# Kernel optimization log

Hardware: AMD Instinct MI355X
Metric: run time of the kernel (lower is better)

Reference implementation:

```python
import jax, jax.numpy as jnp
import numpy as np

# Dims: B INRs, N probe points, d_in=2 coords, hidden H, out D_OUT, proj P
B, N, D_IN, H, D_OUT, P = 128, 4096, 2, 128, 3, 128
W0_SIREN = 30.0  # SIREN frequency scale
LN_EPS = 1e-5


def setup_inputs() -> dict:
    key = jax.random.key(0)
    ks = jax.random.split(key, 12)
    sn = lambda k, shape, sc: (jax.random.normal(k, shape, dtype=jnp.float32) * sc)
    return {
        # per-sample SIREN params, torch layout: weight [b, in, out, 1], bias [b, out, 1]
        "w0": sn(ks[0], (B, D_IN, H, 1), 1.0 / D_IN),
        "w1": sn(ks[1], (B, H, H, 1), np.sqrt(6.0 / H) / W0_SIREN),
        "w2": sn(ks[2], (B, H, D_OUT, 1), np.sqrt(6.0 / H) / W0_SIREN),
        "b0": sn(ks[3], (B, H, 1), 0.1),
        "b1": sn(ks[4], (B, H, 1), 0.1),
        "b2": sn(ks[5], (B, D_OUT, 1), 0.1),
        # learned probe coordinates, initialized U[-1, 1) as in the module
        "inputs": jax.random.uniform(ks[6], (1, N, D_IN), dtype=jnp.float32, minval=-1.0, maxval=1.0),
        # projection (num_inputs -> proj_dim) + LayerNorm params, one per probed layer (4 total)
        "pw": sn(ks[7], (4, N, P), 1.0 / np.sqrt(N)),
        "pb": jnp.zeros((4, P), jnp.float32),
        "ln_g": jnp.ones((4, P), jnp.float32),
        "ln_b": jnp.zeros((4, P), jnp.float32),
    }


def _layernorm(x, g, b):
    m = jnp.mean(x, axis=-1, keepdims=True)
    v = jnp.mean(jnp.square(x - m), axis=-1, keepdims=True)
    return (x - m) * jax.lax.rsqrt(v + LN_EPS) * g + b


def reference(w0, w1, w2, b0, b1, b2, inputs, pw, pb, ln_g, ln_b):
    b = w0.shape[0]
    x = jnp.broadcast_to(inputs, (b,) + inputs.shape[1:])  # [b, n, d_in]

    def lin(h, W, bb):
        # per-sample linear: [b,n,i] @ [b,i,o] + [b,1,o]
        return jnp.einsum('bni,bio->bno', h, W[..., 0]) + bb[:, None, :, 0]

    h1 = jnp.sin(W0_SIREN * lin(x, w0, b0))   # [b, n, H]
    h2 = jnp.sin(W0_SIREN * lin(h1, w1, b1))  # [b, n, H]
    h3 = lin(h2, w2, b2)                      # [b, n, D_OUT] (last layer: no sine)
    feats = [x, h1, h2, h3]  # probe features per node layer (input coords + activations)

    outs = []
    for i, f in enumerate(feats):
        # permute to [b, dim_i, n], project n -> P, then LayerNorm over P
        z = jnp.einsum('bnd,np->bdp', f, pw[i]) + pb[i]
        outs.append(_layernorm(z, ln_g[i], ln_b[i]))
    return jnp.concatenate(outs, axis=1)  # [b, d_in + H + H + D_OUT, P]
```

## Files before the change

### kernel.cpp

```cpp
#include <hip/hip_runtime.h>
#include <hip/hip_bf16.h>


typedef unsigned short u16;
typedef __attribute__((ext_vector_type(8))) short short8;
typedef __attribute__((ext_vector_type(4))) short short4v;
typedef __attribute__((ext_vector_type(4))) float f32x4;
typedef __attribute__((ext_vector_type(4))) float float4v;

#define DEV __device__ __forceinline__

#define KSC 4.7746482927568605f

DEV float b2f(u16 h){ return __uint_as_float(((unsigned)h) << 16); }
DEV u16 f2b(float f){
  unsigned u = __float_as_uint(f);
  return (u16)((u + 0x7FFFu + ((u >> 16) & 1u)) >> 16);
}
DEV u16 f2b_hw(float f){
  __hip_bfloat16 h = __float2bfloat16(f);
  return __builtin_bit_cast(unsigned short, h);
}
DEV float sin_rev(float r){
#if __has_builtin(__builtin_amdgcn_sinf)
  return __builtin_amdgcn_sinf(r);
#else
  return __sinf(r * 6.283185307179586f);
#endif
}
template<int C> DEV float dpp_add(float x){
  int yi = __builtin_amdgcn_update_dpp(0, __float_as_int(x), C, 0xF, 0xF, true);
  return x + __int_as_float(yi);
}
DEV float sum16(float x){
  x = dpp_add<0x128>(x); x = dpp_add<0x124>(x);
  x = dpp_add<0x122>(x); x = dpp_add<0x121>(x);
  return x;
}

DEV int is_bf16_fmt(const void* lng){ return *(const unsigned*)lng == 0x3F803F80u; }
struct In {
  const float* f; const u16* h; int bf;
  DEV In(const void* p, int b_) : f((const float*)p), h((const u16*)p), bf(b_) {}
  DEV float at(size_t i) const { return bf ? b2f(h[i]) : f[i]; }
};

__global__ __launch_bounds__(256) void k_prep(const void* pwv, const void* inpv,
                                              const void* lngv,
                                              u16* __restrict__ pwT2,
                                              float* __restrict__ xbuf,
                                              float* __restrict__ zpart){
  const int bf = is_bf16_fmt(lngv);
  const int t = threadIdx.x;
  if (blockIdx.x == 256){
    In inp(inpv, bf);
    for (int i = t; i < 8192; i += 256) xbuf[i] = inp.at(i);
    return;
  }
  In pw(pwv, bf);
  const int layer = blockIdx.x >> 6;
  const int nc = blockIdx.x & 63;
  const int n0 = nc * 64;

  if (layer == 0){
    In inp(inpv, bf);
    const int d = t >> 7, p = t & 127;
    float s = 0.f;
#pragma unroll 8
    for (int k = 0; k < 64; k++)
      s = fmaf(inp.at((size_t)(n0 + k) * 2 + d),
               pw.at((size_t)(n0 + k) * 128 + p), s);
    zpart[(size_t)nc * 384 + d * 128 + p] = s;
    return;
  }

  __shared__ u16 tile[64 * 129];
  const size_t base = ((size_t)layer * 4096 + n0) * 128;
#pragma unroll
  for (int k = 0; k < 32; k++){
    int idx = k * 256 + t, n = idx >> 7, p = idx & 127;
    tile[n * 129 + p] = f2b(pw.at(base + (size_t)n * 128 + p));
  }
  if (layer == 3 && t < 128){
    float s = 0.f;
#pragma unroll 8
    for (int k = 0; k < 64; k++)
      s += pw.at(base + (size_t)k * 128 + t);
    zpart[(size_t)nc * 384 + 256 + t] = s;
  }
  __syncthreads();
  u16* dst = pwT2 + ((size_t)(layer - 1) * 128 + nc * 2) * 4096;
#pragma unroll
  for (int k = 0; k < 32; k++){
    int o = k * 256 + t;
    int frag = (o >> 3) & 511, j = o & 7;
    int p = ((frag >> 6) << 4) | ((frag >> 2) & 15);
    int nn = ((o >> 12) << 5) | ((frag & 3) << 3) | j;
    dst[o] = tile[nn * 129 + p];
  }
}

__global__ __launch_bounds__(384)
void k_zs2(const float* __restrict__ zpart, float* __restrict__ zs){
  const int t = threadIdx.x;
  float s = 0.f;
  for (int c = 0; c < 64; c++) s += zpart[(size_t)c * 384 + t];
  zs[t] = s;
}

#define S_NK 136
#define S_T  40

template<bool PARTIAL>
__global__ __launch_bounds__(512, 2)
void k_main(const void* w0v, const void* w1v, const void* w2v,
            const void* b0v, const void* b1v, const void* b2v,
            const void* pbv, const void* lgv, const void* lbv,
            const u16* __restrict__ pwTg, const float* __restrict__ xbuf,
            const float* __restrict__ zs,
            float* __restrict__ outp, int TS){
  __shared__ __align__(16) u16 sh1nk[32 * S_NK];
  __shared__ __align__(16) u16 sh1T[128 * S_T];
  __shared__ __align__(16) u16 sh2T[2][128 * S_T];
  __shared__ float sW2[512];
  __shared__ float sb2[4];
  __shared__ float sPB[512], sG[512], sBB[512];

  float* sP1 = (float*)sh1nk;
  float* sP2 = (float*)sh1T;
  float* sM  = (float*)sh2T;
  float* sI  = (float*)sh2T + 512;

  const int bf = is_bf16_fmt(lgv);
  In w0(w0v, bf), w1(w1v, bf), w2(w2v, bf), b0(b0v, bf), b1(b1v, bf),
     b2(b2v, bf), pb(pbv, bf), lg(lgv, bf), lb(lbv, bf);

  const int t = threadIdx.x;
  const int b = blockIdx.x & 127, sseg = blockIdx.x >> 7;
  const int lane = t & 63, wave = t >> 6, quad = lane >> 4, r16 = lane & 15;
  const int oo = wave * 16 + r16;

  if (t >= 256 && t < 384){
    int i = t - 256;
    sW2[i * 4 + 0] = w2.at(((size_t)b * 128 + i) * 3 + 0);
    sW2[i * 4 + 1] = w2.at(((size_t)b * 128 + i) * 3 + 1);
    sW2[i * 4 + 2] = w2.at(((size_t)b * 128 + i) * 3 + 2);
    sW2[i * 4 + 3] = 0.f;
  }
  if (t < 4) sb2[t] = (t < 3) ? b2.at(b * 3 + t) : 0.f;
  sPB[t] = pb.at(t); sG[t] = lg.at(t); sBB[t] = lb.at(t);

  const int p1n = t >> 4, p1hb = (t & 15) * 8;
  float w00[8], w01[8], b00[8];
#pragma unroll
  for (int j = 0; j < 8; j++){
    w00[j] = w0.at((size_t)b * 256 + p1hb + j) * KSC;
    w01[j] = w0.at((size_t)b * 256 + 128 + p1hb + j) * KSC;
    b00[j] = b0.at((size_t)b * 128 + p1hb + j) * KSC;
  }
  const int p2h = t & 127, p2nb = (t >> 7) * 8;
  const float q00 = w0.at((size_t)b * 256 + p2h) * KSC;
  const float q01 = w0.at((size_t)b * 256 + 128 + p2h) * KSC;
  const float qb0 = b0.at((size_t)b * 128 + p2h) * KSC;
  const float bias1k = b1.at((size_t)b * 128 + oo) * KSC;

  short8 w1f[4];
#pragma unroll
  for (int ks = 0; ks < 4; ks++){
#pragma unroll
    for (int j = 0; j < 8; j++)
      w1f[ks][j] = (short)f2b(w1.at((size_t)b * 16384 +
                                    (size_t)(ks * 32 + quad * 8 + j) * 128 + oo));
  }

  const int frag = wave * 64 + r16 * 4 + quad;
  const u16* bsrc = pwTg + (size_t)frag * 8;

  const f32x4 zz = {0.f,0.f,0.f,0.f};
  f32x4 az1[8], az2[8], ay[8];
#pragma unroll
  for (int i = 0; i < 8; i++){ az1[i] = zz; az2[i] = zz; ay[i] = zz; }

  const int nb0 = sseg * TS;
  short8 bbc[3];
#pragma unroll
  for (int L = 0; L < 3; L++)
    bbc[L] = *(const short8*)(bsrc + ((size_t)L * 128 + nb0) * 4096);
  short8 bb2p = bbc[1], bb3p = bbc[2];
  float2 xp1 = *(const float2*)(xbuf + (size_t)(nb0 * 32 + p1n) * 2);

  __syncthreads();

  int cb = 0;
  for (int nt = 0; nt < TS; nt++){
    const int n0 = (sseg * TS + nt) * 32;

    float4v xq[4];
#pragma unroll
    for (int q = 0; q < 4; q++)
      xq[q] = *(const float4v*)(xbuf + (size_t)(n0 + p2nb) * 2 + q * 4);
    {
      short8 v;
#pragma unroll
      for (int j = 0; j < 8; j++){
        float a = fmaf(xp1.y, w01[j], fmaf(xp1.x, w00[j], b00[j]));
        a -= rintf(a);
        v[j] = (short)f2b_hw(sin_rev(a));
      }
      *(short8*)&sh1nk[p1n * S_NK + p1hb] = v;
    }
    {
      short8 v;
#pragma unroll
      for (int j = 0; j < 8; j++){
        float x0 = xq[j >> 1][(j & 1) * 2], x1 = xq[j >> 1][(j & 1) * 2 + 1];
        float a = fmaf(x1, q01, fmaf(x0, q00, qb0));
        a -= rintf(a);
        v[j] = (short)f2b_hw(sin_rev(a));
      }
      *(short8*)&sh1T[p2h * S_T + p2nb] = v;
    }
    if (nt){
      const u16* s2p = sh2T[cb ^ 1];
#pragma unroll
      for (int mb = 0; mb < 8; mb++){
        short8 a = *(const short8*)&s2p[(mb * 16 + r16) * S_T + quad * 8];
        az2[mb] = __builtin_amdgcn_mfma_f32_16x16x32_bf16(a, bb2p, az2[mb], 0, 0, 0);
        ay[mb]  = __builtin_amdgcn_mfma_f32_16x16x32_bf16(a, bb3p, ay[mb], 0, 0, 0);
      }
    }
    __syncthreads();

    {
      const int nn = (nt + 1 < TS) ? nt + 1 : nt;
      const int nbn = sseg * TS + nn;
      short8 bbn[3];
#pragma unroll
      for (int L = 0; L < 3; L++)
        bbn[L] = *(const short8*)(bsrc + ((size_t)L * 128 + nbn) * 4096);
      float2 xp1n = *(const float2*)(xbuf + (size_t)(nbn * 32 + p1n) * 2);

      f32x4 h0 = zz, h1a = zz;
#pragma unroll
      for (int ks = 0; ks < 4; ks++){
        h0  = __builtin_amdgcn_mfma_f32_16x16x32_bf16(
                *(short8*)&sh1nk[r16 * S_NK + ks * 32 + quad * 8], w1f[ks], h0, 0, 0, 0);
        h1a = __builtin_amdgcn_mfma_f32_16x16x32_bf16(
                *(short8*)&sh1nk[(16 + r16) * S_NK + ks * 32 + quad * 8], w1f[ks], h1a, 0, 0, 0);
      }
#pragma unroll
      for (int mb = 0; mb < 8; mb++)
        az1[mb] = __builtin_amdgcn_mfma_f32_16x16x32_bf16(
                    *(short8*)&sh1T[(mb * 16 + r16) * S_T + quad * 8],
                    bbc[0], az1[mb], 0, 0, 0);
      {
        short4v v;
#pragma unroll
        for (int r = 0; r < 4; r++){
          float a = fmaf(h0[r], KSC, bias1k); a -= rintf(a);
          v[r] = (short)f2b_hw(sin_rev(a));
        }
        *(short4v*)&sh2T[cb][oo * S_T + quad * 4] = v;
#pragma unroll
        for (int r = 0; r < 4; r++){
          float a = fmaf(h1a[r], KSC, bias1k); a -= rintf(a);
          v[r] = (short)f2b_hw(sin_rev(a));
        }
        *(short4v*)&sh2T[cb][oo * S_T + 16 + quad * 4] = v;
      }

      bb2p = bbc[1]; bb3p = bbc[2];
#pragma unroll
      for (int L = 0; L < 3; L++) bbc[L] = bbn[L];
      xp1 = xp1n;
    }
    __syncthreads();
    cb ^= 1;
  }

  {
    const u16* s2p = sh2T[cb ^ 1];
#pragma unroll
    for (int mb = 0; mb < 8; mb++){
      short8 a = *(const short8*)&s2p[(mb * 16 + r16) * S_T + quad * 8];
      az2[mb] = __builtin_amdgcn_mfma_f32_16x16x32_bf16(a, bb2p, az2[mb], 0, 0, 0);
      ay[mb]  = __builtin_amdgcn_mfma_f32_16x16x32_bf16(a, bb3p, ay[mb], 0, 0, 0);
    }
  }

  const int p = oo;
  float z3v[3];
#pragma unroll
  for (int d = 0; d < 3; d++){
    float a = 0.f;
#pragma unroll
    for (int mb = 0; mb < 8; mb++)
#pragma unroll
      for (int r = 0; r < 4; r++)
        a = fmaf(sW2[(mb * 16 + quad * 4 + r) * 4 + d], ay[mb][r], a);
    a += __shfl_xor(a, 16, 64); a += __shfl_xor(a, 32, 64);
    z3v[d] = a;
  }
  if (!PARTIAL){
    const float S3v = zs[256 + p];
#pragma unroll
    for (int d = 0; d < 3; d++) z3v[d] += sb2[d] * S3v;
  }

  if (PARTIAL){
    float* zp = outp + ((size_t)(sseg * 128 + b)) * 261 * 128;
    if (quad == 0){
#pragma unroll
      for (int d = 0; d < 3; d++) zp[(size_t)(258 + d) * 128 + p] = z3v[d];
    }
#pragma unroll
    for (int mb = 0; mb < 8; mb++)
#pragma unroll
      for (int r = 0; r < 4; r++){
        int drow = mb * 16 + quad * 4 + r;
        zp[(size_t)(2 + drow) * 128 + p]   = az1[mb][r];
        zp[(size_t)(130 + drow) * 128 + p] = az2[mb][r];
      }
    return;
  }

  const float pb0v = sPB[p],       pb1v = sPB[128 + p];
  const float pb2v = sPB[256 + p], pb3v = sPB[384 + p];

  auto rowsum = [&](float v, int row, bool wr){
    float s1 = sum16(v), s2 = sum16(v * v);
    if (wr && r16 == 0){ sP1[row * 8 + wave] = s1; sP2[row * 8 + wave] = s2; }
  };
#pragma unroll
  for (int mb = 0; mb < 8; mb++)
#pragma unroll
    for (int r = 0; r < 4; r++)
      rowsum(az1[mb][r] + pb1v, 2 + mb * 16 + quad * 4 + r, true);
#pragma unroll
  for (int mb = 0; mb < 8; mb++)
#pragma unroll
    for (int r = 0; r < 4; r++)
      rowsum(az2[mb][r] + pb2v, 130 + mb * 16 + quad * 4 + r, true);
#pragma unroll
  for (int d = 0; d < 3; d++) rowsum(z3v[d] + pb3v, 258 + d, quad == 0);
  __syncthreads();

  if (t < 2){
    float s1 = 0.f, s2 = 0.f;
    for (int pp = 0; pp < 128; pp++){
      float v = zs[t * 128 + pp] + sPB[pp];
      s1 += v; s2 += v * v;
    }
    float m = s1 * (1.f / 128.f);
    float var = fmaf(-m, m, s2 * (1.f / 128.f));
    sM[t] = m;
    sI[t] = rsqrtf(fmaxf(var, 0.f) + 1e-5f);
  } else if (t < 261){
    float s1 = 0.f, s2 = 0.f;
#pragma unroll
    for (int w = 0; w < 8; w++){ s1 += sP1[t * 8 + w]; s2 += sP2[t * 8 + w]; }
    float m = s1 * (1.f / 128.f);
    float var = fmaf(-m, m, s2 * (1.f / 128.f));
    sM[t] = m;
    sI[t] = rsqrtf(fmaxf(var, 0.f) + 1e-5f);
  }
  __syncthreads();

  const size_t ob = (size_t)b * 261 * 128;
  auto emit = [&](float v, int row, int grp){
    outp[ob + (size_t)row * 128 + p] =
      (v - sM[row]) * sI[row] * sG[grp * 128 + p] + sBB[grp * 128 + p];
  };
  if (quad == 0){
#pragma unroll
    for (int r = 0; r < 2; r++) emit(zs[r * 128 + p] + pb0v, r, 0);
#pragma unroll
    for (int d = 0; d < 3; d++) emit(z3v[d] + pb3v, 258 + d, 3);
  }
#pragma unroll
  for (int mb = 0; mb < 8; mb++)
#pragma unroll
    for (int r = 0; r < 4; r++)
      emit(az1[mb][r] + pb1v, 2 + mb * 16 + quad * 4 + r, 1);
#pragma unroll
  for (int mb = 0; mb < 8; mb++)
#pragma unroll
    for (int r = 0; r < 4; r++)
      emit(az2[mb][r] + pb2v, 130 + mb * 16 + quad * 4 + r, 2);
}

__global__ __launch_bounds__(256)
void k_ln(const float* __restrict__ zp, const void* pbv, const void* lgv,
          const void* lbv, const void* b2v, const float* __restrict__ zpart,
          float* __restrict__ out, int split){
  const int bf = is_bf16_fmt(lgv);
  In pb(pbv, bf), lg(lgv, bf), lb(lbv, bf), b2(b2v, bf);
  const int lane = threadIdx.x & 63;
  const int row = blockIdx.x * 4 + (threadIdx.x >> 6);
  const int b = row / 261, d = row % 261;
  const int grp = (d < 2) ? 0 : (d < 130) ? 1 : (d < 258) ? 2 : 3;
  const int p0 = lane * 2;
  float v0 = pb.at(grp * 128 + p0), v1 = pb.at(grp * 128 + p0 + 1);
  if (d < 2){
    float s0 = 0.f, s1z = 0.f;
    for (int c = 0; c < 64; c++){
      s0  += zpart[(size_t)c * 384 + d * 128 + p0];
      s1z += zpart[(size_t)c * 384 + d * 128 + p0 + 1];
    }
    v0 += s0;
    v1 += s1z;
  } else {
    for (int s2 = 0; s2 < split; s2++){
      const float* zr = zp + ((size_t)(s2 * 128 + b) * 261 + d) * 128;
      v0 += zr[p0]; v1 += zr[p0 + 1];
    }
    if (d >= 258){
      float s0 = 0.f, s1z = 0.f;
      for (int c = 0; c < 64; c++){
        s0  += zpart[(size_t)c * 384 + 256 + p0];
        s1z += zpart[(size_t)c * 384 + 256 + p0 + 1];
      }
      float bb = b2.at((size_t)b * 3 + (d - 258));
      v0 = fmaf(bb, s0, v0);
      v1 = fmaf(bb, s1z, v1);
    }
  }
  float s1 = v0 + v1, s2s = v0 * v0 + v1 * v1;
#pragma unroll
  for (int o = 1; o < 64; o <<= 1){
    s1 += __shfl_xor(s1, o, 64);
    s2s += __shfl_xor(s2s, o, 64);
  }
  float m = s1 * (1.f / 128.f);
  float var = fmaf(-m, m, s2s * (1.f / 128.f));
  float inv = rsqrtf(fmaxf(var, 0.f) + 1e-5f);
  float2 o2;
  o2.x = (v0 - m) * inv * lg.at(grp * 128 + p0)     + lb.at(grp * 128 + p0);
  o2.y = (v1 - m) * inv * lg.at(grp * 128 + p0 + 1) + lb.at(grp * 128 + p0 + 1);
  *(float2*)(out + (size_t)row * 128 + p0) = o2;
}

extern "C" void kernel_launch(void* const* d_in, const int* in_sizes, int n_in,
                              void* d_out, int out_size, void* d_ws, size_t ws_size,
                              hipStream_t stream){
  const void* w0  = d_in[0];
  const void* w1  = d_in[1];
  const void* w2  = d_in[2];
  const void* b0  = d_in[3];
  const void* b1  = d_in[4];
  const void* b2  = d_in[5];
  const void* inp = d_in[6];
  const void* pw  = d_in[7];
  const void* pb  = d_in[8];
  const void* lng = d_in[9];
  const void* lnb = d_in[10];
  float* out = (float*)d_out;

  char* ws = (char*)d_ws;
  u16* pwT2    = (u16*)ws;
  float* xbuf  = (float*)(ws + 3145728);
  float* zs    = (float*)(ws + 3145728 + 32768);
  float* zpart = (float*)(ws + 3145728 + 32768 + 2048);
  const size_t zoff = 3145728 + 32768 + 2048 + 98304;
  float* zp = (float*)(ws + zoff);
  const size_t seg = (size_t)128 * 261 * 128 * 4;

  const int split = (ws_size >= zoff + 2 * seg) ? 2 : 1;

  k_prep<<<257, 256, 0, stream>>>(pw, inp, lng, pwT2, xbuf, zpart);
  if (split == 2){
    k_main<true><<<256, 512, 0, stream>>>(w0, w1, w2, b0, b1, b2,
        pb, lng, lnb, pwT2, xbuf, zs, zp, 64);
    k_ln<<<(128 * 261) / 4, 256, 0, stream>>>(zp, pb, lng, lnb, b2, zpart, out, 2);
  } else {
    k_zs2<<<1, 384, 0, stream>>>(zpart, zs);
    k_main<false><<<128, 512, 0, stream>>>(w0, w1, w2, b0, b1, b2,
        pb, lng, lnb, pwT2, xbuf, zs, out, 128);
  }
}
```

Before: 218.6 us.

## Retile main MFMA loop to 2x4 wave grid and always use separate LN kernel

Each wave now owns a 64-row by 32-column tile, using two B fragments per layer, instead of a full 128-row strip with one fragment. Each A fragment read from shared memory now feeds two MFMAs, which roughly halves LDS A-fragment reads at the cost of twice the global B loads. The fused LayerNorm path inside k_main is removed, so k_main always writes partial projections that k_ln normalises, including the split=1 case. The z3 contributions are reduced across the two row-waves through shared memory.

```diff
diff --git a/kernel.cpp b/kernel.cpp
--- a/kernel.cpp
+++ b/kernel.cpp
@@ -27,15 +27,6 @@
 #else
   return __sinf(r * 6.283185307179586f);
 #endif
-}
-template<int C> DEV float dpp_add(float x){
-  int yi = __builtin_amdgcn_update_dpp(0, __float_as_int(x), C, 0xF, 0xF, true);
-  return x + __int_as_float(yi);
-}
-DEV float sum16(float x){
-  x = dpp_add<0x128>(x); x = dpp_add<0x124>(x);
-  x = dpp_add<0x122>(x); x = dpp_add<0x121>(x);
-  return x;
 }
 
 DEV int is_bf16_fmt(const void* lng){ return *(const unsigned*)lng == 0x3F803F80u; }
@@ -100,45 +91,29 @@
   }
 }
 
-__global__ __launch_bounds__(384)
-void k_zs2(const float* __restrict__ zpart, float* __restrict__ zs){
-  const int t = threadIdx.x;
-  float s = 0.f;
-  for (int c = 0; c < 64; c++) s += zpart[(size_t)c * 384 + t];
-  zs[t] = s;
-}
-
 #define S_NK 136
 #define S_T  40
 
-template<bool PARTIAL>
 __global__ __launch_bounds__(512, 2)
 void k_main(const void* w0v, const void* w1v, const void* w2v,
-            const void* b0v, const void* b1v, const void* b2v,
-            const void* pbv, const void* lgv, const void* lbv,
+            const void* b0v, const void* b1v, const void* lgv,
             const u16* __restrict__ pwTg, const float* __restrict__ xbuf,
-            const float* __restrict__ zs,
             float* __restrict__ outp, int TS){
   __shared__ __align__(16) u16 sh1nk[32 * S_NK];
   __shared__ __align__(16) u16 sh1T[128 * S_T];
   __shared__ __align__(16) u16 sh2T[2][128 * S_T];
   __shared__ float sW2[512];
-  __shared__ float sb2[4];
-  __shared__ float sPB[512], sG[512], sBB[512];
-
-  float* sP1 = (float*)sh1nk;
-  float* sP2 = (float*)sh1T;
-  float* sM  = (float*)sh2T;
-  float* sI  = (float*)sh2T + 512;
+
+  float* sZ3 = (float*)sh1nk;
 
   const int bf = is_bf16_fmt(lgv);
-  In w0(w0v, bf), w1(w1v, bf), w2(w2v, bf), b0(b0v, bf), b1(b1v, bf),
-     b2(b2v, bf), pb(pbv, bf), lg(lgv, bf), lb(lbv, bf);
+  In w0(w0v, bf), w1(w1v, bf), w2(w2v, bf), b0(b0v, bf), b1(b1v, bf);
 
   const int t = threadIdx.x;
   const int b = blockIdx.x & 127, sseg = blockIdx.x >> 7;
   const int lane = t & 63, wave = t >> 6, quad = lane >> 4, r16 = lane & 15;
   const int oo = wave * 16 + r16;
+  const int wr = wave >> 2, wc = wave & 3;
 
   if (t >= 256 && t < 384){
     int i = t - 256;
@@ -147,8 +122,6 @@
     sW2[i * 4 + 2] = w2.at(((size_t)b * 128 + i) * 3 + 2);
     sW2[i * 4 + 3] = 0.f;
   }
-  if (t < 4) sb2[t] = (t < 3) ? b2.at(b * 3 + t) : 0.f;
-  sPB[t] = pb.at(t); sG[t] = lg.at(t); sBB[t] = lb.at(t);
 
   const int p1n = t >> 4, p1hb = (t & 15) * 8;
   float w00[8], w01[8], b00[8];
@@ -173,8 +146,8 @@
                                     (size_t)(ks * 32 + quad * 8 + j) * 128 + oo));
   }
 
-  const int frag = wave * 64 + r16 * 4 + quad;
-  const u16* bsrc = pwTg + (size_t)frag * 8;
+  const u16* bsrc0 = pwTg + (size_t)((wc * 2    ) * 64 + r16 * 4 + quad) * 8;
+  const u16* bsrc1 = pwTg + (size_t)((wc * 2 + 1) * 64 + r16 * 4 + quad) * 8;
 
   const f32x4 zz = {0.f,0.f,0.f,0.f};
   f32x4 az1[8], az2[8], ay[8];
@@ -182,11 +155,14 @@
   for (int i = 0; i < 8; i++){ az1[i] = zz; az2[i] = zz; ay[i] = zz; }
 
   const int nb0 = sseg * TS;
-  short8 bbc[3];
-#pragma unroll
-  for (int L = 0; L < 3; L++)
-    bbc[L] = *(const short8*)(bsrc + ((size_t)L * 128 + nb0) * 4096);
-  short8 bb2p = bbc[1], bb3p = bbc[2];
+  short8 bbc[3][2];
+#pragma unroll
+  for (int L = 0; L < 3; L++){
+    bbc[L][0] = *(const short8*)(bsrc0 + ((size_t)L * 128 + nb0) * 4096);
+    bbc[L][1] = *(const short8*)(bsrc1 + ((size_t)L * 128 + nb0) * 4096);
+  }
+  short8 bb2p0 = bbc[1][0], bb2p1 = bbc[1][1];
+  short8 bb3p0 = bbc[2][0], bb3p1 = bbc[2][1];
   float2 xp1 = *(const float2*)(xbuf + (size_t)(nb0 * 32 + p1n) * 2);
 
   __syncthreads();
@@ -223,10 +199,12 @@
     if (nt){
       const u16* s2p = sh2T[cb ^ 1];
 #pragma unroll
-      for (int mb = 0; mb < 8; mb++){
-        short8 a = *(const short8*)&s2p[(mb * 16 + r16) * S_T + quad * 8];
-        az2[mb] = __builtin_amdgcn_mfma_f32_16x16x32_bf16(a, bb2p, az2[mb], 0, 0, 0);
-        ay[mb]  = __builtin_amdgcn_mfma_f32_16x16x32_bf16(a, bb3p, ay[mb], 0, 0, 0);
+      for (int m = 0; m < 4; m++){
+        short8 a = *(const short8*)&s2p[(wr * 64 + m * 16 + r16) * S_T + quad * 8];
+        az2[m*2+0] = __builtin_amdgcn_mfma_f32_16x16x32_bf16(a, bb2p0, az2[m*2+0], 0, 0, 0);
+        az2[m*2+1] = __builtin_amdgcn_mfma_f32_16x16x32_bf16(a, bb2p1, az2[m*2+1], 0, 0, 0);
+        ay[m*2+0]  = __builtin_amdgcn_mfma_f32_16x16x32_bf16(a, bb3p0, ay[m*2+0], 0, 0, 0);
+        ay[m*2+1]  = __builtin_amdgcn_mfma_f32_16x16x32_bf16(a, bb3p1, ay[m*2+1], 0, 0, 0);
       }
     }
     __syncthreads();
@@ -234,10 +212,12 @@
     {
       const int nn = (nt + 1 < TS) ? nt + 1 : nt;
       const int nbn = sseg * TS + nn;
-      short8 bbn[3];
-#pragma unroll
-      for (int L = 0; L < 3; L++)
-        bbn[L] = *(const short8*)(bsrc + ((size_t)L * 128 + nbn) * 4096);
+      short8 bbn[3][2];
+#pragma unroll
+      for (int L = 0; L < 3; L++){
+        bbn[L][0] = *(const short8*)(bsrc0 + ((size_t)L * 128 + nbn) * 4096);
+        bbn[L][1] = *(const short8*)(bsrc1 + ((size_t)L * 128 + nbn) * 4096);
+      }
       float2 xp1n = *(const float2*)(xbuf + (size_t)(nbn * 32 + p1n) * 2);
 
       f32x4 h0 = zz, h1a = zz;
@@ -249,10 +229,11 @@
                 *(short8*)&sh1nk[(16 + r16) * S_NK + ks * 32 + quad * 8], w1f[ks], h1a, 0, 0, 0);
       }
 #pragma unroll
-      for (int mb = 0; mb < 8; mb++)
-        az1[mb] = __builtin_amdgcn_mfma_f32_16x16x32_bf16(
-                    *(short8*)&sh1T[(mb * 16 + r16) * S_T + quad * 8],
-                    bbc[0], az1[mb], 0, 0, 0);
+      for (int m = 0; m < 4; m++){
+        short8 a = *(const short8*)&sh1T[(wr * 64 + m * 16 + r16) * S_T + quad * 8];
+        az1[m*2+0] = __builtin_amdgcn_mfma_f32_16x16x32_bf16(a, bbc[0][0], az1[m*2+0], 0, 0, 0);
+        az1[m*2+1] = __builtin_amdgcn_mfma_f32_16x16x32_bf16(a, bbc[0][1], az1[m*2+1], 0, 0, 0);
+      }
       {
         short4v v;
 #pragma unroll
@@ -269,9 +250,10 @@
         *(short4v*)&sh2T[cb][oo * S_T + 16 + quad * 4] = v;
       }
 
-      bb2p = bbc[1]; bb3p = bbc[2];
-#pragma unroll
-      for (int L = 0; L < 3; L++) bbc[L] = bbn[L];
+      bb2p0 = bbc[1][0]; bb2p1 = bbc[1][1];
+      bb3p0 = bbc[2][0]; bb3p1 = bbc[2][1];
+#pragma unroll
+      for (int L = 0; L < 3; L++){ bbc[L][0] = bbn[L][0]; bbc[L][1] = bbn[L][1]; }
       xp1 = xp1n;
     }
     __syncthreads();
@@ -281,112 +263,57 @@
   {
     const u16* s2p = sh2T[cb ^ 1];
 #pragma unroll
-    for (int mb = 0; mb < 8; mb++){
-      short8 a = *(const short8*)&s2p[(mb * 16 + r16) * S_T + quad * 8];
-      az2[mb] = __builtin_amdgcn_mfma_f32_16x16x32_bf16(a, bb2p, az2[mb], 0, 0, 0);
-      ay[mb]  = __builtin_amdgcn_mfma_f32_16x16x32_bf16(a, bb3p, ay[mb], 0, 0, 0);
-    }
-  }
-
-  const int p = oo;
-  float z3v[3];
-#pragma unroll
-  for (int d = 0; d < 3; d++){
-    float a = 0.f;
-#pragma unroll
-    for (int mb = 0; mb < 8; mb++)
-#pragma unroll
-      for (int r = 0; r < 4; r++)
-        a = fmaf(sW2[(mb * 16 + quad * 4 + r) * 4 + d], ay[mb][r], a);
-    a += __shfl_xor(a, 16, 64); a += __shfl_xor(a, 32, 64);
-    z3v[d] = a;
-  }
-  if (!PARTIAL){
-    const float S3v = zs[256 + p];
-#pragma unroll
-    for (int d = 0; d < 3; d++) z3v[d] += sb2[d] * S3v;
-  }
-
-  if (PARTIAL){
-    float* zp = outp + ((size_t)(sseg * 128 + b)) * 261 * 128;
-    if (quad == 0){
-#pragma unroll
-      for (int d = 0; d < 3; d++) zp[(size_t)(258 + d) * 128 + p] = z3v[d];
-    }
-#pragma unroll
-    for (int mb = 0; mb < 8; mb++)
+    for (int m = 0; m < 4; m++){
+      short8 a = *(const short8*)&s2p[(wr * 64 + m * 16 + r16) * S_T + quad * 8];
+      az2[m*2+0] = __builtin_amdgcn_mfma_f32_16x16x32_bf16(a, bb2p0, az2[m*2+0], 0, 0, 0);
+      az2[m*2+1] = __builtin_amdgcn_mfma_f32_16x16x32_bf16(a, bb2p1, az2[m*2+1], 0, 0, 0);
+      ay[m*2+0]  = __builtin_amdgcn_mfma_f32_16x16x32_bf16(a, bb3p0, ay[m*2+0], 0, 0, 0);
+      ay[m*2+1]  = __builtin_amdgcn_mfma_f32_16x16x32_bf16(a, bb3p1, ay[m*2+1], 0, 0, 0);
+    }
+  }
+
+  float z3p[3][2];
+#pragma unroll
+  for (int dd = 0; dd < 3; dd++){
+#pragma unroll
+    for (int n = 0; n < 2; n++){
+      float a = 0.f;
+#pragma unroll
+      for (int m = 0; m < 4; m++)
+#pragma unroll
+        for (int r = 0; r < 4; r++)
+          a = fmaf(sW2[(wr * 64 + m * 16 + quad * 4 + r) * 4 + dd], ay[m*2+n][r], a);
+      a += __shfl_xor(a, 16, 64); a += __shfl_xor(a, 32, 64);
+      z3p[dd][n] = a;
+    }
+  }
+  if (lane < 16){
+#pragma unroll
+    for (int dd = 0; dd < 3; dd++)
+#pragma unroll
+      for (int n = 0; n < 2; n++)
+        sZ3[((wr * 4 + wc) * 3 + dd) * 32 + n * 16 + r16] = z3p[dd][n];
+  }
+
+  float* zp = outp + ((size_t)(sseg * 128 + b)) * 261 * 128;
+#pragma unroll
+  for (int m = 0; m < 4; m++)
+#pragma unroll
+    for (int n = 0; n < 2; n++)
 #pragma unroll
       for (int r = 0; r < 4; r++){
-        int drow = mb * 16 + quad * 4 + r;
-        zp[(size_t)(2 + drow) * 128 + p]   = az1[mb][r];
-        zp[(size_t)(130 + drow) * 128 + p] = az2[mb][r];
-      }
-    return;
-  }
-
-  const float pb0v = sPB[p],       pb1v = sPB[128 + p];
-  const float pb2v = sPB[256 + p], pb3v = sPB[384 + p];
-
-  auto rowsum = [&](float v, int row, bool wr){
-    float s1 = sum16(v), s2 = sum16(v * v);
-    if (wr && r16 == 0){ sP1[row * 8 + wave] = s1; sP2[row * 8 + wave] = s2; }
-  };
-#pragma unroll
-  for (int mb = 0; mb < 8; mb++)
-#pragma unroll
-    for (int r = 0; r < 4; r++)
-      rowsum(az1[mb][r] + pb1v, 2 + mb * 16 + quad * 4 + r, true);
-#pragma unroll
-  for (int mb = 0; mb < 8; mb++)
-#pragma unroll
-    for (int r = 0; r < 4; r++)
-      rowsum(az2[mb][r] + pb2v, 130 + mb * 16 + quad * 4 + r, true);
-#pragma unroll
-  for (int d = 0; d < 3; d++) rowsum(z3v[d] + pb3v, 258 + d, quad == 0);
+        int drow = wr * 64 + m * 16 + quad * 4 + r;
+        int pcol = wc * 32 + n * 16 + r16;
+        zp[(size_t)(2 + drow) * 128 + pcol]   = az1[m*2+n][r];
+        zp[(size_t)(130 + drow) * 128 + pcol] = az2[m*2+n][r];
+      }
   __syncthreads();
-
-  if (t < 2){
-    float s1 = 0.f, s2 = 0.f;
-    for (int pp = 0; pp < 128; pp++){
-      float v = zs[t * 128 + pp] + sPB[pp];
-      s1 += v; s2 += v * v;
-    }
-    float m = s1 * (1.f / 128.f);
-    float var = fmaf(-m, m, s2 * (1.f / 128.f));
-    sM[t] = m;
-    sI[t] = rsqrtf(fmaxf(var, 0.f) + 1e-5f);
-  } else if (t < 261){
-    float s1 = 0.f, s2 = 0.f;
-#pragma unroll
-    for (int w = 0; w < 8; w++){ s1 += sP1[t * 8 + w]; s2 += sP2[t * 8 + w]; }
-    float m = s1 * (1.f / 128.f);
-    float var = fmaf(-m, m, s2 * (1.f / 128.f));
-    sM[t] = m;
-    sI[t] = rsqrtf(fmaxf(var, 0.f) + 1e-5f);
-  }
-  __syncthreads();
-
-  const size_t ob = (size_t)b * 261 * 128;
-  auto emit = [&](float v, int row, int grp){
-    outp[ob + (size_t)row * 128 + p] =
-      (v - sM[row]) * sI[row] * sG[grp * 128 + p] + sBB[grp * 128 + p];
-  };
-  if (quad == 0){
-#pragma unroll
-    for (int r = 0; r < 2; r++) emit(zs[r * 128 + p] + pb0v, r, 0);
-#pragma unroll
-    for (int d = 0; d < 3; d++) emit(z3v[d] + pb3v, 258 + d, 3);
-  }
-#pragma unroll
-  for (int mb = 0; mb < 8; mb++)
-#pragma unroll
-    for (int r = 0; r < 4; r++)
-      emit(az1[mb][r] + pb1v, 2 + mb * 16 + quad * 4 + r, 1);
-#pragma unroll
-  for (int mb = 0; mb < 8; mb++)
-#pragma unroll
-    for (int r = 0; r < 4; r++)
-      emit(az2[mb][r] + pb2v, 130 + mb * 16 + quad * 4 + r, 2);
+  if (t < 384){
+    int dd = t >> 7, p = t & 127, wcc = p >> 5, pl = p & 31;
+    float v = sZ3[((0 * 4 + wcc) * 3 + dd) * 32 + pl]
+            + sZ3[((1 * 4 + wcc) * 3 + dd) * 32 + pl];
+    zp[(size_t)(258 + dd) * 128 + p] = v;
+  }
 }
 
 __global__ __launch_bounds__(256)
@@ -459,22 +386,15 @@
   char* ws = (char*)d_ws;
   u16* pwT2    = (u16*)ws;
   float* xbuf  = (float*)(ws + 3145728);
-  float* zs    = (float*)(ws + 3145728 + 32768);
-  float* zpart = (float*)(ws + 3145728 + 32768 + 2048);
-  const size_t zoff = 3145728 + 32768 + 2048 + 98304;
+  float* zpart = (float*)(ws + 3145728 + 32768);
+  const size_t zoff = 3145728 + 32768 + 98304;
   float* zp = (float*)(ws + zoff);
   const size_t seg = (size_t)128 * 261 * 128 * 4;
 
   const int split = (ws_size >= zoff + 2 * seg) ? 2 : 1;
 
   k_prep<<<257, 256, 0, stream>>>(pw, inp, lng, pwT2, xbuf, zpart);
-  if (split == 2){
-    k_main<true><<<256, 512, 0, stream>>>(w0, w1, w2, b0, b1, b2,
-        pb, lng, lnb, pwT2, xbuf, zs, zp, 64);
-    k_ln<<<(128 * 261) / 4, 256, 0, stream>>>(zp, pb, lng, lnb, b2, zpart, out, 2);
-  } else {
-    k_zs2<<<1, 384, 0, stream>>>(zpart, zs);
-    k_main<false><<<128, 512, 0, stream>>>(w0, w1, w2, b0, b1, b2,
-        pb, lng, lnb, pwT2, xbuf, zs, out, 128);
-  }
-}
+  k_main<<<128 * split, 512, 0, stream>>>(w0, w1, w2, b0, b1,
+      lng, pwT2, xbuf, zp, 4096 / (32 * split));
+  k_ln<<<(128 * 261) / 4, 256, 0, stream>>>(zp, pb, lng, lnb, b2, zpart, out, split);
+}
```

Result: slower. 224.3 us (+2.6%).
